# Kernel optimization log

Measured on AMD Instinct MI355X. Metric: run time of the kernel, lower is better.

## Reference

```python
import jax, jax.numpy as jnp
import numpy as np

N = 50000   # nodes
E = 800000  # edges
DIN, DH, DOUT = 128, 128, 128


def _w(k, o, i):
    return jax.random.normal(k, (o, i), jnp.float32) * (1.0 / np.sqrt(i))


def setup_inputs() -> dict:
    key = jax.random.key(0)
    ks = jax.random.split(key, 16)
    return {
        "x": jax.random.normal(ks[0], (N, DIN), jnp.float32),
        "edge_index": jax.random.randint(ks[1], (2, E), 0, N, dtype=jnp.int64),
        # conv1 = GraphSAGE(DIN, DH, num_layers=2): two SAGEConv layers
        "W1l": _w(ks[2], DH, DIN), "W1r": _w(ks[3], DH, DIN), "b1": jnp.zeros((DH,), jnp.float32),
        "W2l": _w(ks[4], DH, DH),  "W2r": _w(ks[5], DH, DH),  "b2": jnp.zeros((DH,), jnp.float32),
        # conv2 = GraphSAGE(DH, DOUT, num_layers=2)
        "W3l": _w(ks[6], DOUT, DH),   "W3r": _w(ks[7], DOUT, DH),   "b3": jnp.zeros((DOUT,), jnp.float32),
        "W4l": _w(ks[8], DOUT, DOUT), "W4r": _w(ks[9], DOUT, DOUT), "b4": jnp.zeros((DOUT,), jnp.float32),
        # final fc
        "Wfc": _w(ks[10], DOUT, DOUT), "bfc": jnp.zeros((DOUT,), jnp.float32),
    }


def _sage(x, src, dst, Wl, Wr, b):
    # PyG SAGEConv (aggr='mean'): out = lin_l(mean_{j in N(i)} x_j) + lin_r(x_i)
    agg = jax.ops.segment_sum(x[src], dst, num_segments=N)          # [N, F]
    cnt = jax.ops.segment_sum(jnp.ones((src.shape[0],), x.dtype), dst, num_segments=N)
    mean = agg / jnp.maximum(cnt, 1.0)[:, None]                     # isolated nodes -> 0
    return mean @ Wl.T + x @ Wr.T + b


def reference(x, edge_index, W1l, W1r, b1, W2l, W2r, b2,
              W3l, W3r, b3, W4l, W4r, b4, Wfc, bfc):
    src, dst = edge_index[0], edge_index[1]
    h = _sage(x, src, dst, W1l, W1r, b1)
    h = jax.nn.relu(h)                        # inter-layer act inside conv1
    h = _sage(h, src, dst, W2l, W2r, b2)
    h = jax.nn.relu(h)                        # F.relu(self.conv1(...))
    h = _sage(h, src, dst, W3l, W3r, b3)
    h = jax.nn.relu(h)                        # inter-layer act inside conv2
    h = _sage(h, src, dst, W4l, W4r, b4)
    h = jax.nn.relu(h)                        # F.relu(self.conv2(...))
    return h @ Wfc.T + bfc
```

## Files before the change

kernel.cpp:

```cpp
#include <hip/hip_runtime.h>

#define DF 128
#define SCAN_TILE 2048
#define SHP 136

typedef __attribute__((ext_vector_type(8))) short bf16x8;
typedef __attribute__((ext_vector_type(4))) float f32x4;

__device__ __forceinline__ ushort f2b(float f) {
    uint u = __float_as_uint(f);
    u += 0x7FFF + ((u >> 16) & 1);
    return (ushort)(u >> 16);
}
__device__ __forceinline__ float blo(uint v) { return __uint_as_float(v << 16); }
__device__ __forceinline__ float bhi(uint v) { return __uint_as_float(v & 0xFFFF0000u); }
__device__ __forceinline__ uint pk(float lo, float hi) {
    return (uint)f2b(lo) | ((uint)f2b(hi) << 16);
}


__global__ void count_kernel(const int* __restrict__ dst, int* __restrict__ cnt, int E) {
    int e = blockIdx.x * blockDim.x + threadIdx.x;
    if (e < E) atomicAdd(&cnt[dst[e]], 1);
}

__global__ __launch_bounds__(256) void scan_reduce(const int* __restrict__ cnt,
                                                   int* __restrict__ bsum, int N) {
    __shared__ int sw[4];
    const int tid = threadIdx.x, lane = tid & 63, wid = tid >> 6;
    const int base = blockIdx.x * SCAN_TILE + tid * 8;
    int s = 0;
    #pragma unroll
    for (int j = 0; j < 8; ++j) { int i = base + j; if (i < N) s += cnt[i]; }
    #pragma unroll
    for (int off = 1; off < 64; off <<= 1) s += __shfl_xor(s, off);
    if (lane == 0) sw[wid] = s;
    __syncthreads();
    if (tid == 0) bsum[blockIdx.x] = sw[0] + sw[1] + sw[2] + sw[3];
}

__global__ __launch_bounds__(64) void scan_blocksums(int* __restrict__ bsum, int nb,
                                                     int* __restrict__ row_start, int N) {
    const int lane = threadIdx.x;
    int v = (lane < nb) ? bsum[lane] : 0;
    int incl = v;
    #pragma unroll
    for (int off = 1; off < 64; off <<= 1) {
        int t = __shfl_up(incl, off);
        if (lane >= off) incl += t;
    }
    if (lane < nb) bsum[lane] = incl - v;
    if (lane == 63) row_start[N] = incl;
}

__global__ __launch_bounds__(256) void scan_apply(const int* __restrict__ cnt,
                                                  const int* __restrict__ bsum,
                                                  int* __restrict__ row_start,
                                                  int* __restrict__ cur,
                                                  float* __restrict__ inv, int N) {
    __shared__ int sw[4];
    const int tid = threadIdx.x, lane = tid & 63, wid = tid >> 6;
    const int base = blockIdx.x * SCAN_TILE + tid * 8;
    int v[8];
    int tsum = 0;
    #pragma unroll
    for (int j = 0; j < 8; ++j) {
        int i = base + j;
        v[j] = (i < N) ? cnt[i] : 0;
        tsum += v[j];
    }
    int incl = tsum;
    #pragma unroll
    for (int off = 1; off < 64; off <<= 1) {
        int t = __shfl_up(incl, off);
        if (lane >= off) incl += t;
    }
    if (lane == 63) sw[wid] = incl;
    __syncthreads();
    int woff = 0;
    #pragma unroll
    for (int k = 0; k < 4; ++k) woff += (k < wid) ? sw[k] : 0;
    int run = bsum[blockIdx.x] + woff + (incl - tsum);
    #pragma unroll
    for (int j = 0; j < 8; ++j) {
        int i = base + j;
        if (i < N) {
            row_start[i] = run;
            cur[i]       = run;
            inv[i]       = 1.0f / fmaxf((float)v[j], 1.0f);
        }
        run += v[j];
    }
}

__global__ void place_kernel(const int* __restrict__ src, const int* __restrict__ dst,
                             int* __restrict__ cur, ushort* __restrict__ col, int E) {
    int e = blockIdx.x * blockDim.x + threadIdx.x;
    if (e < E) {
        int p = atomicAdd(&cur[dst[e]], 1);
        col[p] = (ushort)src[e];
    }
}


__global__ void cvt_x_kernel(const float* __restrict__ in, ushort* __restrict__ out, int n4) {
    int i = blockIdx.x * blockDim.x + threadIdx.x;
    if (i < n4) {
        float4 v = *reinterpret_cast<const float4*>(in + (long long)i * 4);
        uint2 p;
        p.x = pk(v.x, v.y);
        p.y = pk(v.z, v.w);
        *reinterpret_cast<uint2*>(out + (long long)i * 4) = p;
    }
}

struct WPtrs { const float* p[9]; };

__global__ void cvt_w_kernel(WPtrs w, ushort* __restrict__ out) {
    int m = blockIdx.y;
    int i = blockIdx.x * 256 + threadIdx.x;
    out[m * 16384 + i] = f2b(w.p[m][i]);
}


__global__ __launch_bounds__(256) void aggregate_kernel(
        const ushort* __restrict__ H,
        const int* __restrict__ row_start, const ushort* __restrict__ col,
        const float* __restrict__ inv, ushort* __restrict__ M, int N) {
    const int node = blockIdx.x * 4 + (threadIdx.x >> 6);
    const int lane = threadIdx.x & 63;
    if (node >= N) return;
    const int s = row_start[node], e = row_start[node + 1];
    const int half = lane >> 5, l32 = lane & 31;
    const uint2* __restrict__ Hu = reinterpret_cast<const uint2*>(H);
    float a0 = 0.f, a1 = 0.f, a2 = 0.f, a3 = 0.f;
    int j = s;
    for (; j + 8 <= e; j += 8) {
        int n0 = (int)col[j + 0 + half];
        int n1 = (int)col[j + 2 + half];
        int n2 = (int)col[j + 4 + half];
        int n3 = (int)col[j + 6 + half];
        uint2 v0 = Hu[n0 * 32 + l32];
        uint2 v1 = Hu[n1 * 32 + l32];
        uint2 v2 = Hu[n2 * 32 + l32];
        uint2 v3 = Hu[n3 * 32 + l32];
        a0 += blo(v0.x); a1 += bhi(v0.x); a2 += blo(v0.y); a3 += bhi(v0.y);
        a0 += blo(v1.x); a1 += bhi(v1.x); a2 += blo(v1.y); a3 += bhi(v1.y);
        a0 += blo(v2.x); a1 += bhi(v2.x); a2 += blo(v2.y); a3 += bhi(v2.y);
        a0 += blo(v3.x); a1 += bhi(v3.x); a2 += blo(v3.y); a3 += bhi(v3.y);
    }
    for (; j + 2 <= e; j += 2) {
        int n0 = (int)col[j + half];
        uint2 v0 = Hu[n0 * 32 + l32];
        a0 += blo(v0.x); a1 += bhi(v0.x); a2 += blo(v0.y); a3 += bhi(v0.y);
    }
    if (j < e && half == 0) {
        int n0 = (int)col[j];
        uint2 v0 = Hu[n0 * 32 + l32];
        a0 += blo(v0.x); a1 += bhi(v0.x); a2 += blo(v0.y); a3 += bhi(v0.y);
    }
    a0 += __shfl_xor(a0, 32);
    a1 += __shfl_xor(a1, 32);
    a2 += __shfl_xor(a2, 32);
    a3 += __shfl_xor(a3, 32);
    if (half == 0) {
        const float iv = inv[node];
        uint2 p;
        p.x = pk(a0 * iv, a1 * iv);
        p.y = pk(a2 * iv, a3 * iv);
        reinterpret_cast<uint2*>(M + (long long)node * DF)[l32] = p;
    }
}

__device__ __forceinline__ void stage2(const ushort* __restrict__ g1,
                                       const ushort* __restrict__ g2,
                                       ushort* s1, ushort* s2, int tid) {
    bf16x8 v1[4], v2[4];
    #pragma unroll
    for (int q = 0; q < 4; ++q) {
        int idx = q * 256 + tid;
        int row = idx >> 4, ch = (idx & 15) * 8;
        v1[q] = *reinterpret_cast<const bf16x8*>(g1 + row * DF + ch);
        v2[q] = *reinterpret_cast<const bf16x8*>(g2 + row * DF + ch);
    }
    #pragma unroll
    for (int q = 0; q < 4; ++q) {
        int idx = q * 256 + tid;
        int row = idx >> 4, ch = (idx & 15) * 8;
        *reinterpret_cast<bf16x8*>(s1 + row * SHP + ch) = v1[q];
        *reinterpret_cast<bf16x8*>(s2 + row * SHP + ch) = v2[q];
    }
}


__global__ __launch_bounds__(256) void gemm_mfma(
    const ushort* __restrict__ A1,
    const ushort* __restrict__ A2,
    const ushort* __restrict__ W1,
    const ushort* __restrict__ W2,
    const float* __restrict__ bias,
    ushort* __restrict__ outB,
    int n)
{
    __shared__ ushort sA1[64 * SHP];
    __shared__ ushort sA2[64 * SHP];

    const int tid  = threadIdx.x;
    const int lane = tid & 63;
    const int w    = tid >> 6;
    const int n0   = blockIdx.x * 64;
    const int r16  = lane & 15;
    const int kq   = (lane >> 4) * 8;

    stage2(A1 + (long long)n0 * DF, A2 + (long long)n0 * DF, sA1, sA2, tid);
    __syncthreads();

    f32x4 acc[4][2];
    #pragma unroll
    for (int i = 0; i < 4; ++i)
        #pragma unroll
        for (int j = 0; j < 2; ++j) acc[i][j] = (f32x4){0.f, 0.f, 0.f, 0.f};

    #pragma unroll
    for (int pass = 0; pass < 2; ++pass) {
        const ushort* sA = pass ? sA2 : sA1;
        const ushort* W  = pass ? W2 : W1;
        #pragma unroll
        for (int kk = 0; kk < 4; ++kk) {
            const int k0 = kk * 32 + kq;
            bf16x8 b[2];
            #pragma unroll
            for (int ct = 0; ct < 2; ++ct) {
                int o = w * 32 + ct * 16 + r16;
                b[ct] = *reinterpret_cast<const bf16x8*>(W + o * DF + k0);
            }
            #pragma unroll
            for (int rt = 0; rt < 4; ++rt) {
                bf16x8 a = *reinterpret_cast<const bf16x8*>(sA + (rt * 16 + r16) * SHP + k0);
                #pragma unroll
                for (int ct = 0; ct < 2; ++ct)
                    acc[rt][ct] = __builtin_amdgcn_mfma_f32_16x16x32_bf16(a, b[ct], acc[rt][ct], 0, 0, 0);
            }
        }
    }

    #pragma unroll
    for (int rt = 0; rt < 4; ++rt) {
        #pragma unroll
        for (int ct = 0; ct < 2; ++ct) {
            const int c = w * 32 + ct * 16 + r16;
            const float bv = bias[c];
            #pragma unroll
            for (int r = 0; r < 4; ++r) {
                int row = n0 + rt * 16 + (lane >> 4) * 4 + r;
                if (row < n) {
                    float v = fmaxf(acc[rt][ct][r] + bv, 0.0f);
                    outB[(long long)row * DF + c] = f2b(v);
                }
            }
        }
    }
}


__global__ __launch_bounds__(256) void gemm_mfma_fc(
    const ushort* __restrict__ A1,
    const ushort* __restrict__ A2,
    const ushort* __restrict__ W1,
    const ushort* __restrict__ W2,
    const float* __restrict__ bias1,
    const ushort* __restrict__ Wf,
    const float* __restrict__ biasf,
    float* __restrict__ out,
    int n)
{
    __shared__ ushort sA1[64 * SHP];
    __shared__ ushort sA2[64 * SHP];

    const int tid  = threadIdx.x;
    const int lane = tid & 63;
    const int w    = tid >> 6;
    const int n0   = blockIdx.x * 64;
    const int r16  = lane & 15;
    const int kq   = (lane >> 4) * 8;

    stage2(A1 + (long long)n0 * DF, A2 + (long long)n0 * DF, sA1, sA2, tid);
    __syncthreads();

    f32x4 acc[4][2];
    #pragma unroll
    for (int i = 0; i < 4; ++i)
        #pragma unroll
        for (int j = 0; j < 2; ++j) acc[i][j] = (f32x4){0.f, 0.f, 0.f, 0.f};

    #pragma unroll
    for (int pass = 0; pass < 2; ++pass) {
        const ushort* sA = pass ? sA2 : sA1;
        const ushort* W  = pass ? W2 : W1;
        #pragma unroll
        for (int kk = 0; kk < 4; ++kk) {
            const int k0 = kk * 32 + kq;
            bf16x8 b[2];
            #pragma unroll
            for (int ct = 0; ct < 2; ++ct) {
                int o = w * 32 + ct * 16 + r16;
                b[ct] = *reinterpret_cast<const bf16x8*>(W + o * DF + k0);
            }
            #pragma unroll
            for (int rt = 0; rt < 4; ++rt) {
                bf16x8 a = *reinterpret_cast<const bf16x8*>(sA + (rt * 16 + r16) * SHP + k0);
                #pragma unroll
                for (int ct = 0; ct < 2; ++ct)
                    acc[rt][ct] = __builtin_amdgcn_mfma_f32_16x16x32_bf16(a, b[ct], acc[rt][ct], 0, 0, 0);
            }
        }
    }

    __syncthreads();

    #pragma unroll
    for (int rt = 0; rt < 4; ++rt) {
        #pragma unroll
        for (int ct = 0; ct < 2; ++ct) {
            const int c = w * 32 + ct * 16 + r16;
            const float bv = bias1[c];
            #pragma unroll
            for (int r = 0; r < 4; ++r) {
                int lrow = rt * 16 + (lane >> 4) * 4 + r;
                sA1[lrow * SHP + c] = f2b(fmaxf(acc[rt][ct][r] + bv, 0.0f));
            }
        }
    }
    __syncthreads();

    f32x4 acc2[4][2];
    #pragma unroll
    for (int i = 0; i < 4; ++i)
        #pragma unroll
        for (int j = 0; j < 2; ++j) acc2[i][j] = (f32x4){0.f, 0.f, 0.f, 0.f};

    #pragma unroll
    for (int kk = 0; kk < 4; ++kk) {
        const int k0 = kk * 32 + kq;
        bf16x8 b[2];
        #pragma unroll
        for (int ct = 0; ct < 2; ++ct) {
            int o = w * 32 + ct * 16 + r16;
            b[ct] = *reinterpret_cast<const bf16x8*>(Wf + o * DF + k0);
        }
        #pragma unroll
        for (int rt = 0; rt < 4; ++rt) {
            bf16x8 a = *reinterpret_cast<const bf16x8*>(&sA1[(rt * 16 + r16) * SHP + k0]);
            #pragma unroll
            for (int ct = 0; ct < 2; ++ct)
                acc2[rt][ct] = __builtin_amdgcn_mfma_f32_16x16x32_bf16(a, b[ct], acc2[rt][ct], 0, 0, 0);
        }
    }

    #pragma unroll
    for (int rt = 0; rt < 4; ++rt) {
        #pragma unroll
        for (int ct = 0; ct < 2; ++ct) {
            const int c = w * 32 + ct * 16 + r16;
            const float bv = biasf[c];
            #pragma unroll
            for (int r = 0; r < 4; ++r) {
                int row = n0 + rt * 16 + (lane >> 4) * 4 + r;
                if (row < n)
                    out[(long long)row * DF + c] = acc2[rt][ct][r] + bv;
            }
        }
    }
}

extern "C" void kernel_launch(void* const* d_in, const int* in_sizes, int n_in,
                              void* d_out, int out_size, void* d_ws, size_t ws_size,
                              hipStream_t stream) {
    const float* x  = (const float*)d_in[0];
    const int*   ei = (const int*)d_in[1];
    const int N = in_sizes[0] / DF;
    const int E = in_sizes[1] / 2;
    const int* src = ei;
    const int* dst = ei + E;

    const float* b1  = (const float*)d_in[4];
    const float* b2  = (const float*)d_in[7];
    const float* b3  = (const float*)d_in[10];
    const float* b4  = (const float*)d_in[13];
    const float* bfc = (const float*)d_in[15];

    float* out = (float*)d_out;

    char* ws = (char*)d_ws;
    size_t off = 0;
    auto alloc = [&](size_t bytes) { char* p = ws + off; off = (off + bytes + 255) & ~(size_t)255; return p; };
    int*    cnt       = (int*)   alloc((size_t)N * 4);
    int*    row_start = (int*)   alloc((size_t)(N + 1) * 4);
    int*    cur       = (int*)   alloc((size_t)N * 4);
    float*  inv       = (float*) alloc((size_t)N * 4);
    int*    bsum      = (int*)   alloc(256 * 4);
    ushort* col       = (ushort*)alloc((size_t)E * 2);
    ushort* Xb        = (ushort*)alloc((size_t)N * DF * 2);
    ushort* M         = (ushort*)alloc((size_t)N * DF * 2);
    ushort* H         = (ushort*)alloc((size_t)N * DF * 2);
    ushort* Wb        = (ushort*)alloc((size_t)9 * 16384 * 2);
    (void)alloc(16384);

    hipMemsetAsync(cnt, 0, (size_t)N * 4, stream);
    count_kernel<<<dim3((E + 255) / 256), dim3(256), 0, stream>>>(dst, cnt, E);
    const int nb = (N + SCAN_TILE - 1) / SCAN_TILE;
    scan_reduce<<<dim3(nb), dim3(256), 0, stream>>>(cnt, bsum, N);
    scan_blocksums<<<dim3(1), dim3(64), 0, stream>>>(bsum, nb, row_start, N);
    scan_apply<<<dim3(nb), dim3(256), 0, stream>>>(cnt, bsum, row_start, cur, inv, N);
    place_kernel<<<dim3((E + 255) / 256), dim3(256), 0, stream>>>(src, dst, cur, col, E);

    const int n4 = N * DF / 4;
    cvt_x_kernel<<<dim3((n4 + 255) / 256), dim3(256), 0, stream>>>(x, Xb, n4);
    WPtrs wp;
    wp.p[0] = (const float*)d_in[2];  wp.p[1] = (const float*)d_in[3];
    wp.p[2] = (const float*)d_in[5];  wp.p[3] = (const float*)d_in[6];
    wp.p[4] = (const float*)d_in[8];  wp.p[5] = (const float*)d_in[9];
    wp.p[6] = (const float*)d_in[11]; wp.p[7] = (const float*)d_in[12];
    wp.p[8] = (const float*)d_in[14];
    cvt_w_kernel<<<dim3(64, 9), dim3(256), 0, stream>>>(wp, Wb);

    const int agrid = (N + 3) / 4;
    const int ggrid = (N + 63) / 64;

    aggregate_kernel<<<dim3(agrid), dim3(256), 0, stream>>>(Xb, row_start, col, inv, M, N);
    gemm_mfma<<<dim3(ggrid), dim3(256), 0, stream>>>(M, Xb, Wb + 0*16384, Wb + 1*16384, b1, H, N);
    aggregate_kernel<<<dim3(agrid), dim3(256), 0, stream>>>(H, row_start, col, inv, M, N);
    gemm_mfma<<<dim3(ggrid), dim3(256), 0, stream>>>(M, H, Wb + 2*16384, Wb + 3*16384, b2, H, N);
    aggregate_kernel<<<dim3(agrid), dim3(256), 0, stream>>>(H, row_start, col, inv, M, N);
    gemm_mfma<<<dim3(ggrid), dim3(256), 0, stream>>>(M, H, Wb + 4*16384, Wb + 5*16384, b3, H, N);
    aggregate_kernel<<<dim3(agrid), dim3(256), 0, stream>>>(H, row_start, col, inv, M, N);
    gemm_mfma_fc<<<dim3(ggrid), dim3(256), 0, stream>>>(M, H, Wb + 6*16384, Wb + 7*16384, b4,
                                                        Wb + 8*16384, bfc, out, N);
}
```

Before: 308.4 us.

## Fuse neighbor aggregation into SAGE GEMM kernels and merge prep kernels

Neighbor mean aggregation now runs inside each GEMM block: each wave gathers 16 nodes into shared memory, so the intermediate M buffer is no longer written to and re-read from global memory. H and M are ping-ponged because a layer cannot overwrite its input while other blocks are still gathering from it. The count, x-conversion and weight-conversion kernels are merged into one launch to cut launch overhead. In exchange, the gather grid drops from about 12500 blocks to about 780, and each wave walks 16 nodes one after another, which lowers the memory-level parallelism available to hide gather latency.

```diff
diff --git a/kernel.cpp b/kernel.cpp
--- a/kernel.cpp
+++ b/kernel.cpp
@@ -19,10 +19,32 @@
 }
 
 
-__global__ void count_kernel(const int* __restrict__ dst, int* __restrict__ cnt, int E) {
-    int e = blockIdx.x * blockDim.x + threadIdx.x;
-    if (e < E) atomicAdd(&cnt[dst[e]], 1);
-}
+struct WPtrs { const float* p[9]; };
+
+__global__ void prep_kernel(const int* __restrict__ dst, int* __restrict__ cnt, int E, int CB,
+                            const float* __restrict__ x, ushort* __restrict__ Xb, int n4, int XB,
+                            WPtrs w, ushort* __restrict__ Wb) {
+    const int b = blockIdx.x, tid = threadIdx.x;
+    if (b < CB) {
+        int e = b * 256 + tid;
+        if (e < E) atomicAdd(&cnt[dst[e]], 1);
+    } else if (b < CB + XB) {
+        int i = (b - CB) * 256 + tid;
+        if (i < n4) {
+            float4 v = *reinterpret_cast<const float4*>(x + (long long)i * 4);
+            uint2 p;
+            p.x = pk(v.x, v.y);
+            p.y = pk(v.z, v.w);
+            *reinterpret_cast<uint2*>(Xb + (long long)i * 4) = p;
+        }
+    } else {
+        int q = b - CB - XB;
+        int m = q >> 6;
+        int i = (q & 63) * 256 + tid;
+        Wb[m * 16384 + i] = f2b(w.p[m][i]);
+    }
+}
+
 
 __global__ __launch_bounds__(256) void scan_reduce(const int* __restrict__ cnt,
                                                    int* __restrict__ bsum, int N) {
@@ -103,99 +125,80 @@
 }
 
 
-__global__ void cvt_x_kernel(const float* __restrict__ in, ushort* __restrict__ out, int n4) {
-    int i = blockIdx.x * blockDim.x + threadIdx.x;
-    if (i < n4) {
-        float4 v = *reinterpret_cast<const float4*>(in + (long long)i * 4);
-        uint2 p;
-        p.x = pk(v.x, v.y);
-        p.y = pk(v.z, v.w);
-        *reinterpret_cast<uint2*>(out + (long long)i * 4) = p;
-    }
-}
-
-struct WPtrs { const float* p[9]; };
-
-__global__ void cvt_w_kernel(WPtrs w, ushort* __restrict__ out) {
-    int m = blockIdx.y;
-    int i = blockIdx.x * 256 + threadIdx.x;
-    out[m * 16384 + i] = f2b(w.p[m][i]);
-}
-
-
-__global__ __launch_bounds__(256) void aggregate_kernel(
-        const ushort* __restrict__ H,
+__device__ __forceinline__ void gather16(
+        const ushort* __restrict__ Hsrc,
         const int* __restrict__ row_start, const ushort* __restrict__ col,
-        const float* __restrict__ inv, ushort* __restrict__ M, int N) {
-    const int node = blockIdx.x * 4 + (threadIdx.x >> 6);
-    const int lane = threadIdx.x & 63;
-    if (node >= N) return;
-    const int s = row_start[node], e = row_start[node + 1];
+        const float* __restrict__ inv, ushort* sA1,
+        int n0, int w, int lane, int n) {
     const int half = lane >> 5, l32 = lane & 31;
-    const uint2* __restrict__ Hu = reinterpret_cast<const uint2*>(H);
-    float a0 = 0.f, a1 = 0.f, a2 = 0.f, a3 = 0.f;
-    int j = s;
-    for (; j + 8 <= e; j += 8) {
-        int n0 = (int)col[j + 0 + half];
-        int n1 = (int)col[j + 2 + half];
-        int n2 = (int)col[j + 4 + half];
-        int n3 = (int)col[j + 6 + half];
-        uint2 v0 = Hu[n0 * 32 + l32];
-        uint2 v1 = Hu[n1 * 32 + l32];
-        uint2 v2 = Hu[n2 * 32 + l32];
-        uint2 v3 = Hu[n3 * 32 + l32];
-        a0 += blo(v0.x); a1 += bhi(v0.x); a2 += blo(v0.y); a3 += bhi(v0.y);
-        a0 += blo(v1.x); a1 += bhi(v1.x); a2 += blo(v1.y); a3 += bhi(v1.y);
-        a0 += blo(v2.x); a1 += bhi(v2.x); a2 += blo(v2.y); a3 += bhi(v2.y);
-        a0 += blo(v3.x); a1 += bhi(v3.x); a2 += blo(v3.y); a3 += bhi(v3.y);
-    }
-    for (; j + 2 <= e; j += 2) {
-        int n0 = (int)col[j + half];
-        uint2 v0 = Hu[n0 * 32 + l32];
-        a0 += blo(v0.x); a1 += bhi(v0.x); a2 += blo(v0.y); a3 += bhi(v0.y);
-    }
-    if (j < e && half == 0) {
-        int n0 = (int)col[j];
-        uint2 v0 = Hu[n0 * 32 + l32];
-        a0 += blo(v0.x); a1 += bhi(v0.x); a2 += blo(v0.y); a3 += bhi(v0.y);
-    }
-    a0 += __shfl_xor(a0, 32);
-    a1 += __shfl_xor(a1, 32);
-    a2 += __shfl_xor(a2, 32);
-    a3 += __shfl_xor(a3, 32);
-    if (half == 0) {
-        const float iv = inv[node];
-        uint2 p;
-        p.x = pk(a0 * iv, a1 * iv);
-        p.y = pk(a2 * iv, a3 * iv);
-        reinterpret_cast<uint2*>(M + (long long)node * DF)[l32] = p;
-    }
-}
-
-__device__ __forceinline__ void stage2(const ushort* __restrict__ g1,
-                                       const ushort* __restrict__ g2,
-                                       ushort* s1, ushort* s2, int tid) {
-    bf16x8 v1[4], v2[4];
+    const uint2* __restrict__ Hu = reinterpret_cast<const uint2*>(Hsrc);
+    for (int nd = 0; nd < 16; ++nd) {
+        const int node = n0 + w * 16 + nd;
+        float a0 = 0.f, a1 = 0.f, a2 = 0.f, a3 = 0.f;
+        float iv = 0.f;
+        if (node < n) {
+            const int s = row_start[node], e = row_start[node + 1];
+            int j = s;
+            for (; j + 8 <= e; j += 8) {
+                int m0 = (int)col[j + 0 + half];
+                int m1 = (int)col[j + 2 + half];
+                int m2 = (int)col[j + 4 + half];
+                int m3 = (int)col[j + 6 + half];
+                uint2 v0 = Hu[m0 * 32 + l32];
+                uint2 v1 = Hu[m1 * 32 + l32];
+                uint2 v2 = Hu[m2 * 32 + l32];
+                uint2 v3 = Hu[m3 * 32 + l32];
+                a0 += blo(v0.x); a1 += bhi(v0.x); a2 += blo(v0.y); a3 += bhi(v0.y);
+                a0 += blo(v1.x); a1 += bhi(v1.x); a2 += blo(v1.y); a3 += bhi(v1.y);
+                a0 += blo(v2.x); a1 += bhi(v2.x); a2 += blo(v2.y); a3 += bhi(v2.y);
+                a0 += blo(v3.x); a1 += bhi(v3.x); a2 += blo(v3.y); a3 += bhi(v3.y);
+            }
+            for (; j + 2 <= e; j += 2) {
+                int m0 = (int)col[j + half];
+                uint2 v0 = Hu[m0 * 32 + l32];
+                a0 += blo(v0.x); a1 += bhi(v0.x); a2 += blo(v0.y); a3 += bhi(v0.y);
+            }
+            if (j < e && half == 0) {
+                int m0 = (int)col[j];
+                uint2 v0 = Hu[m0 * 32 + l32];
+                a0 += blo(v0.x); a1 += bhi(v0.x); a2 += blo(v0.y); a3 += bhi(v0.y);
+            }
+            iv = inv[node];
+        }
+        a0 += __shfl_xor(a0, 32);
+        a1 += __shfl_xor(a1, 32);
+        a2 += __shfl_xor(a2, 32);
+        a3 += __shfl_xor(a3, 32);
+        if (half == 0) {
+            uint2 p;
+            p.x = pk(a0 * iv, a1 * iv);
+            p.y = pk(a2 * iv, a3 * iv);
+            *reinterpret_cast<uint2*>(sA1 + (w * 16 + nd) * SHP + l32 * 4) = p;
+        }
+    }
+}
+
+__device__ __forceinline__ void stage_own(const ushort* __restrict__ g,
+                                          ushort* s, int tid) {
+    bf16x8 v[4];
     #pragma unroll
     for (int q = 0; q < 4; ++q) {
         int idx = q * 256 + tid;
         int row = idx >> 4, ch = (idx & 15) * 8;
-        v1[q] = *reinterpret_cast<const bf16x8*>(g1 + row * DF + ch);
-        v2[q] = *reinterpret_cast<const bf16x8*>(g2 + row * DF + ch);
+        v[q] = *reinterpret_cast<const bf16x8*>(g + row * DF + ch);
     }
     #pragma unroll
     for (int q = 0; q < 4; ++q) {
         int idx = q * 256 + tid;
         int row = idx >> 4, ch = (idx & 15) * 8;
-        *reinterpret_cast<bf16x8*>(s1 + row * SHP + ch) = v1[q];
-        *reinterpret_cast<bf16x8*>(s2 + row * SHP + ch) = v2[q];
-    }
-}
-
-
-__global__ __launch_bounds__(256) void gemm_mfma(
-    const ushort* __restrict__ A1,
-    const ushort* __restrict__ A2,
+        *reinterpret_cast<bf16x8*>(s + row * SHP + ch) = v[q];
+    }
+}
+
+__global__ __launch_bounds__(256) void sage_fused(
+    const ushort* __restrict__ Hsrc,
+    const int* __restrict__ row_start, const ushort* __restrict__ col,
+    const float* __restrict__ inv,
     const ushort* __restrict__ W1,
     const ushort* __restrict__ W2,
     const float* __restrict__ bias,
@@ -212,7 +215,8 @@
     const int r16  = lane & 15;
     const int kq   = (lane >> 4) * 8;
 
-    stage2(A1 + (long long)n0 * DF, A2 + (long long)n0 * DF, sA1, sA2, tid);
+    stage_own(Hsrc + (long long)n0 * DF, sA2, tid);
+    gather16(Hsrc, row_start, col, inv, sA1, n0, w, lane, n);
     __syncthreads();
 
     f32x4 acc[4][2];
@@ -263,9 +267,10 @@
 }
 
 
-__global__ __launch_bounds__(256) void gemm_mfma_fc(
-    const ushort* __restrict__ A1,
-    const ushort* __restrict__ A2,
+__global__ __launch_bounds__(256) void sage_fused_fc(
+    const ushort* __restrict__ Hsrc,
+    const int* __restrict__ row_start, const ushort* __restrict__ col,
+    const float* __restrict__ inv,
     const ushort* __restrict__ W1,
     const ushort* __restrict__ W2,
     const float* __restrict__ bias1,
@@ -284,7 +289,8 @@
     const int r16  = lane & 15;
     const int kq   = (lane >> 4) * 8;
 
-    stage2(A1 + (long long)n0 * DF, A2 + (long long)n0 * DF, sA1, sA2, tid);
+    stage_own(Hsrc + (long long)n0 * DF, sA2, tid);
+    gather16(Hsrc, row_start, col, inv, sA1, n0, w, lane, n);
     __syncthreads();
 
     f32x4 acc[4][2];
@@ -401,39 +407,39 @@
     int*    bsum      = (int*)   alloc(256 * 4);
     ushort* col       = (ushort*)alloc((size_t)E * 2);
     ushort* Xb        = (ushort*)alloc((size_t)N * DF * 2);
-    ushort* M         = (ushort*)alloc((size_t)N * DF * 2);
-    ushort* H         = (ushort*)alloc((size_t)N * DF * 2);
+    ushort* Hb        = (ushort*)alloc((size_t)N * DF * 2);
+    ushort* Mb        = (ushort*)alloc((size_t)N * DF * 2);
     ushort* Wb        = (ushort*)alloc((size_t)9 * 16384 * 2);
-    (void)alloc(16384);
+    (void)alloc(65536);
 
     hipMemsetAsync(cnt, 0, (size_t)N * 4, stream);
-    count_kernel<<<dim3((E + 255) / 256), dim3(256), 0, stream>>>(dst, cnt, E);
-    const int nb = (N + SCAN_TILE - 1) / SCAN_TILE;
-    scan_reduce<<<dim3(nb), dim3(256), 0, stream>>>(cnt, bsum, N);
-    scan_blocksums<<<dim3(1), dim3(64), 0, stream>>>(bsum, nb, row_start, N);
-    scan_apply<<<dim3(nb), dim3(256), 0, stream>>>(cnt, bsum, row_start, cur, inv, N);
-    place_kernel<<<dim3((E + 255) / 256), dim3(256), 0, stream>>>(src, dst, cur, col, E);
-
     const int n4 = N * DF / 4;
-    cvt_x_kernel<<<dim3((n4 + 255) / 256), dim3(256), 0, stream>>>(x, Xb, n4);
+    const int CB = (E + 255) / 256;
+    const int XB = (n4 + 255) / 256;
+    const int WB = 9 * 64;
     WPtrs wp;
     wp.p[0] = (const float*)d_in[2];  wp.p[1] = (const float*)d_in[3];
     wp.p[2] = (const float*)d_in[5];  wp.p[3] = (const float*)d_in[6];
     wp.p[4] = (const float*)d_in[8];  wp.p[5] = (const float*)d_in[9];
     wp.p[6] = (const float*)d_in[11]; wp.p[7] = (const float*)d_in[12];
     wp.p[8] = (const float*)d_in[14];
-    cvt_w_kernel<<<dim3(64, 9), dim3(256), 0, stream>>>(wp, Wb);
-
-    const int agrid = (N + 3) / 4;
+    prep_kernel<<<dim3(CB + XB + WB), dim3(256), 0, stream>>>(dst, cnt, E, CB, x, Xb, n4, XB, wp, Wb);
+
+    const int nb = (N + SCAN_TILE - 1) / SCAN_TILE;
+    scan_reduce<<<dim3(nb), dim3(256), 0, stream>>>(cnt, bsum, N);
+    scan_blocksums<<<dim3(1), dim3(64), 0, stream>>>(bsum, nb, row_start, N);
+    scan_apply<<<dim3(nb), dim3(256), 0, stream>>>(cnt, bsum, row_start, cur, inv, N);
+    place_kernel<<<dim3(CB), dim3(256), 0, stream>>>(src, dst, cur, col, E);
+
     const int ggrid = (N + 63) / 64;
 
-    aggregate_kernel<<<dim3(agrid), dim3(256), 0, stream>>>(Xb, row_start, col, inv, M, N);
-    gemm_mfma<<<dim3(ggrid), dim3(256), 0, stream>>>(M, Xb, Wb + 0*16384, Wb + 1*16384, b1, H, N);
-    aggregate_kernel<<<dim3(agrid), dim3(256), 0, stream>>>(H, row_start, col, inv, M, N);
-    gemm_mfma<<<dim3(ggrid), dim3(256), 0, stream>>>(M, H, Wb + 2*16384, Wb + 3*16384, b2, H, N);
-    aggregate_kernel<<<dim3(agrid), dim3(256), 0, stream>>>(H, row_start, col, inv, M, N);
-    gemm_mfma<<<dim3(ggrid), dim3(256), 0, stream>>>(M, H, Wb + 4*16384, Wb + 5*16384, b3, H, N);
-    aggregate_kernel<<<dim3(agrid), dim3(256), 0, stream>>>(H, row_start, col, inv, M, N);
-    gemm_mfma_fc<<<dim3(ggrid), dim3(256), 0, stream>>>(M, H, Wb + 6*16384, Wb + 7*16384, b4,
-                                                        Wb + 8*16384, bfc, out, N);
-}
+    sage_fused<<<dim3(ggrid), dim3(256), 0, stream>>>(Xb, row_start, col, inv,
+                                                      Wb + 0*16384, Wb + 1*16384, b1, Hb, N);
+    sage_fused<<<dim3(ggrid), dim3(256), 0, stream>>>(Hb, row_start, col, inv,
+                                                      Wb + 2*16384, Wb + 3*16384, b2, Mb, N);
+    sage_fused<<<dim3(ggrid), dim3(256), 0, stream>>>(Mb, row_start, col, inv,
+                                                      Wb + 4*16384, Wb + 5*16384, b3, Hb, N);
+    sage_fused_fc<<<dim3(ggrid), dim3(256), 0, stream>>>(Hb, row_start, col, inv,
+                                                         Wb + 6*16384, Wb + 7*16384, b4,
+                                                         Wb + 8*16384, bfc, out, N);
+}
```

Result: slower. 373.1 us (+21.0%).
